# Performance work log

Measured on AMD Instinct MI355X. Metric: run time of the kernel, lower is better.

Reference implementation:

```python
import jax, jax.numpy as jnp
import numpy as np


def _fwd_diffs(x, D, scale):
    # forward difference along each of the first D axes, zero at the end, scaled by x.shape[0]
    outs = []
    for d in range(D):
        pad = [(0, 0)] * x.ndim
        pad[d] = (0, 1)
        outs.append(jnp.pad(jnp.diff(x, axis=d), pad) * scale)
    return jnp.stack(outs, 0)


def _bwd_diffs(p, scale):
    # p: [D, *dims, l]; backward difference of p[i] along axis i with the torch narrow/cat semantics
    outs = []
    for i in range(p.shape[0]):
        pi = p[i]
        head = jax.lax.slice_in_dim(pi, 0, pi.shape[i] - 1, axis=i)
        z = jnp.zeros_like(jax.lax.slice_in_dim(pi, 0, 1, axis=i))
        before = jnp.concatenate([head, z], axis=i)
        after = jnp.concatenate([z, head], axis=i)
        outs.append((before - after) * scale)
    return jnp.stack(outs, 0)


def _solver(f, repeats, l, lmbda, nu):
    dims = list(f.shape)
    H = dims[0]
    D = len(dims) - 1
    res = 1.0 / H
    tauu = res / 6.0
    sigmap = res / (3.0 + l)
    sigmas = 1.0
    proj = l * (l - 1) // 2 + l
    tau = 1.0 / (2.0 + proj / 4.0)
    # (k1,k2) interval combinations and the membership matrix M[K,z] = (k1<=z<=k2)
    combos = np.array([(a, b) for a in range(l) for b in range(a, l)], dtype=np.int32)
    k1 = jnp.asarray(combos[:, 0])
    k2 = jnp.asarray(combos[:, 1])
    zz = np.arange(l)
    M = jnp.asarray(((combos[:, :1] <= zz) & (zz <= combos[:, 1:2])).astype(np.float32))  # [proj, l]

    img = jnp.broadcast_to(f[..., None], tuple(dims) + (l,))
    klf = jnp.arange(1, l + 1, dtype=f.dtype) / l - img  # k/l - f
    u = img
    ubar = img
    px = jnp.zeros((D,) + tuple(dims) + (l,), f.dtype)
    pt = jnp.zeros(tuple(dims) + (l,), f.dtype)
    sx = jnp.zeros((D,) + tuple(dims) + (proj,), f.dtype)
    mux = sx
    mubarx = sx
    nrj = jnp.zeros((), f.dtype)
    h_un = u

    for it in range(int(repeats)):
        # ---- parabola: dual ascent on (px,pt) with closed-form cubic (Cardano) projection ----
        musum = jnp.einsum('...p,pz->...z', mux, M)
        ux = px + sigmap * (_fwd_diffs(ubar, D, H) + musum)
        ut = pt + sigmap * (jnp.pad(jnp.diff(ubar, axis=-1), [(0, 0)] * (ubar.ndim - 1) + [(0, 1)]) * l)
        pen = lmbda * klf * klf
        B = 0.25 * jnp.sum(ux * ux, axis=0) - pen
        mask = ut < B
        y = ut + pen
        norm = jnp.sqrt(jnp.sum(ux * ux, axis=0))
        a = 0.5 * norm                                   # 2*0.25*norm
        b = (2.0 / 3.0) * (1.0 - 0.5 * y)
        sb = jnp.sqrt(jnp.maximum(-b, 0.0))              # sqrt(-b), only used where b<0
        d = jnp.where(b < 0, (a - sb ** 3) * (a + sb ** 3), a * a + b ** 3)
        c = jnp.power(a + jnp.sqrt(jnp.maximum(d, 0.0)), 1.0 / 3.0)
        mask1 = (d >= 0) & (c == 0)
        mask3 = d < 0
        sb3 = jnp.where(sb > 0, sb ** 3, 1.0)
        ratio = jnp.clip(a / sb3, -1.0, 1.0)
        c_safe = jnp.where(c == 0, 1.0, c)
        v = jnp.where(mask1, 0.0,
                      jnp.where(mask3, 2.0 * sb * jnp.cos(jnp.arccos(ratio) / 3.0), c - b / c_safe))
        norm_safe = jnp.where(norm == 0, 1.0, norm)
        px = jnp.where(mask[None],
                       jnp.where((norm == 0)[None], 0.0, (2.0 * v / norm_safe)[None] * ux),
                       ux)
        pt = jnp.where(mask, 0.25 * jnp.sum(px * px, axis=0) - pen, ut)

        # ---- l2 projection of s ----
        mx = sx - sigmas * mubarx
        snorm = jnp.sqrt(jnp.sum(mx * mx, axis=0))
        snorm_safe = jnp.where(snorm == 0, 1.0, snorm)
        sx = jnp.where((snorm > nu * H)[None], mx * nu / snorm_safe[None], mx)

        # ---- mu update: per-(k1,k2) partial sums over the label axis via cumsum ----
        cs = jnp.cumsum(px, axis=-1)
        cs = jnp.pad(cs, [(0, 0)] * (px.ndim - 1) + [(1, 0)])
        t = cs[..., k2 + 1] - cs[..., k1]                # [D, *dims, proj]
        mux_new = mux + tau * (sx - t)
        mubarx = 2.0 * mux_new - mux
        mux = mux_new

        # ---- clipping: primal update with box projection and boundary conditions ----
        if it % 10 == 0:
            h_un = u
        dx = _bwd_diffs(px, H)
        head = pt[..., :-1]
        z = jnp.zeros_like(pt[..., :1])
        dt = (jnp.concatenate([head, z], axis=-1) - jnp.concatenate([z, head], axis=-1)) * l
        Dv = u + tauu * (jnp.sum(dx, axis=0) + dt)
        un = jnp.clip(Dv, 0.0, 1.0)
        un = un.at[..., 0].set(1.0).at[..., l - 1].set(0.0)
        ubar = 2.0 * un - u
        u = un
        if it % 10 == 0:
            nrj = jnp.sum(jnp.abs(u - h_un))
    return u, nrj


def setup_inputs() -> dict:
    key = jax.random.key(0)
    H, W = 256, 256
    f = jax.random.uniform(key, (H, W, 1), dtype=jnp.float32)
    return {"f": f, "repeats": 10, "l": 16, "lmbda": 0.5, "nu": 0.1, "tol": 0.0}


def reference(f, repeats, l, lmbda, nu, tol):
    # tol/early-exit: tol=0 so the torch break never fires; iteration count is fixed at `repeats`.
    u, nrj = _solver(f, repeats, l, lmbda, nu)
    denom = float(np.prod(f.shape[:-1])) * l
    return (u, nrj, nrj / denom, 0)
```

## Files before the change

### kernel.cpp

```cpp
#include <hip/hip_runtime.h>

#define HH 256
#define WW 256
#define NPIX (HH*WW)
#define LL 16
#define NL (NPIX*LL)
#define PP 136
#define PP2 (PP*2)

typedef _Float16 half_t;
typedef __attribute__((ext_vector_type(8))) _Float16 half8;

static constexpr float SIGMAP_F = (float)((1.0/256.0)/(3.0+16.0));
static constexpr float TAUU_F   = (float)((1.0/256.0)/6.0);
static constexpr float TAU_F    = (float)(1.0/36.0);

__device__ __forceinline__ float clampf(float x, float lo, float hi){
    return fminf(fmaxf(x, lo), hi);
}

template<int MODE>
__global__ __launch_bounds__(256) void k_prox(const float* __restrict__ f,
    const half_t* __restrict__ ubar,
    const half_t* __restrict__ pxOld,
    half_t* __restrict__ pxCur,
    half_t* __restrict__ pt,
    const half_t* __restrict__ musum,
    float* __restrict__ nrj)
{
    int tid = blockIdx.x*256 + threadIdx.x;
    if (MODE == 0 && tid == 0) *nrj = 0.0f;
    if (tid >= NL) return;
    int z = tid & (LL-1);
    int n = tid >> 4;
    int i = n >> 8;
    int j = n & (WW-1);

    float ux0, ux1, ut;
    float fv = f[n];
    if (MODE == 0) {
        float g0 = (i < HH-1) ? (f[n + WW] - fv) * 256.0f : 0.0f;
        float g1 = (j < WW-1) ? (f[n + 1]  - fv) * 256.0f : 0.0f;
        ux0 = SIGMAP_F * g0;
        ux1 = SIGMAP_F * g1;
        ut  = 0.0f;
    } else {
        float ub = (float)ubar[tid];
        float g0 = (i < HH-1) ? ((float)ubar[tid + WW*LL] - ub) * 256.0f : 0.0f;
        float g1 = (j < WW-1) ? ((float)ubar[tid + LL]    - ub) * 256.0f : 0.0f;
        float gt = (z < LL-1) ? ((float)ubar[tid + 1]     - ub) * 16.0f  : 0.0f;
        float ms0 = (float)musum[tid];
        float ms1 = (float)musum[NL + tid];
        ux0 = (float)pxOld[tid]      + SIGMAP_F * (g0 + ms0);
        ux1 = (float)pxOld[NL + tid] + SIGMAP_F * (g1 + ms1);
        ut  = (float)pt[tid]         + SIGMAP_F * gt;
    }

    float klf = (float)(z + 1) * 0.0625f - fv;
    float pen = 0.5f * klf * klf;

    float n2 = ux0*ux0 + ux1*ux1;
    float B  = 0.25f * n2 - pen;
    bool mask = ut < B;

    float px0 = ux0, px1 = ux1, ptn = ut;
    if (mask) {
        float y    = ut + pen;
        float norm = sqrtf(n2);
        float a    = 0.5f * norm;
        float b    = (2.0f/3.0f) * (1.0f - 0.5f*y);
        float v;
        if (b < 0.0f) {
            float sb  = sqrtf(-b);
            float sb3 = sb*sb*sb;
            float dd  = (a - sb3)*(a + sb3);
            if (dd < 0.0f) {
                float ratio = clampf(a / sb3, -1.0f, 1.0f);
                v = 2.0f * sb * cosf(acosf(ratio) * (1.0f/3.0f));
            } else {
                float c = cbrtf(a + sqrtf(dd));
                v = (c == 0.0f) ? 0.0f : (c - b/c);
            }
        } else {
            float dd = a*a + b*b*b;
            float c  = cbrtf(a + sqrtf(dd));
            v = (c == 0.0f) ? 0.0f : (c - b/c);
        }
        if (norm == 0.0f) { px0 = 0.0f; px1 = 0.0f; }
        else              { float s = 2.0f*v/norm; px0 = s*ux0; px1 = s*ux1; }
        ptn = 0.25f*(px0*px0 + px1*px1) - pen;
    }
    pxCur[tid]      = (half_t)px0;
    pxCur[NL + tid] = (half_t)px1;
    pt[tid]         = (half_t)ptn;
}

template<int H, int MODE>
__device__ __forceinline__ void do_set(int d, int n, int lane,
    half8 ph0, half8 ph1, half8 pp0, half8 pp1,
    const half_t* __restrict__ muC,
    half_t* __restrict__ muO,
    float* __restrict__ part)
{
    constexpr size_t setbase = (size_t)H * 17 * 2 * NPIX;
    const size_t vb   = setbase + (size_t)n*16 + (size_t)d*8;
    const size_t vb1  = vb + (size_t)16*NPIX;
    const size_t tail = setbase + (size_t)32*NPIX + (size_t)n*2 + (size_t)d;

    half8 mCv0, mCv1, mOv0, mOv1;
    float mCT = 0.0f, mOT = 0.0f;
    if (MODE >= 1) {
        mCv0 = *reinterpret_cast<const half8*>(&muC[vb]);
        mCv1 = *reinterpret_cast<const half8*>(&muC[vb1]);
        mCT  = (float)muC[tail];
    }
    if (MODE == 2) {
        mOv0 = *reinterpret_cast<const half8*>(&muO[vb]);
        mOv1 = *reinterpret_cast<const half8*>(&muO[vb1]);
        mOT  = (float)muO[tail];
    }

    half8 muo0, muo1;
    half_t muoT = (half_t)0.0f;

    float C[LL];
    #pragma unroll
    for (int q = 0; q < LL; ++q) C[q] = 0.0f;

    float tsum = 0.0f, tprev = 0.0f, rsA = 0.0f, rsB = 0.0f;
    #pragma unroll
    for (int q = 0; q < 17; ++q) {
        const int b = (q <= 15-H) ? H + q : q - 1;
        if (q == 0 || q == 16-H) { tsum = 0.0f; tprev = 0.0f; }
        tsum  += (b < 8) ? (float)ph0[b] : (float)ph1[b-8];

        float mn;
        if (MODE == 0) {
            mn = -TAU_F * tsum;
        } else {
            float mC, mO = 0.0f;
            if (q < 8)       { mC=(float)mCv0[q];   if (MODE==2) mO=(float)mOv0[q]; }
            else if (q < 16) { mC=(float)mCv1[q-8]; if (MODE==2) mO=(float)mOv1[q-8]; }
            else             { mC=mCT;              if (MODE==2) mO=mOT; }
            tprev += (b < 8) ? (float)pp0[b] : (float)pp1[b-8];

            float sxp = (mC - mO) * 36.0f + tprev;
            float mx  = sxp - (2.0f*mC - mO);
            float mo  = __shfl_xor(mx, 1);
            float snorm = sqrtf(mx*mx + mo*mo);
            if (snorm > 25.6f) mx *= 0.1f / snorm;
            mn = mC + TAU_F*(mx - tsum);
        }

        if (q < 8)       muo0[q]   = (half_t)mn;
        else if (q < 16) muo1[q-8] = (half_t)mn;
        else             muoT      = (half_t)mn;

        if (q <= 15-H) rsA += mn; else rsB += mn;
        C[b] += mn;
    }

    *reinterpret_cast<half8*>(&muO[vb])  = muo0;
    *reinterpret_cast<half8*>(&muO[vb1]) = muo1;
    muO[tail] = muoT;

    float m = 0.0f;
    #pragma unroll
    for (int z = 0; z < LL; ++z) {
        if (z == H)    m += rsA;
        if (z == 15-H) m += rsB;
        if (z >= 1)    m -= C[z-1];
        part[H*1024 + z*64 + lane] = m;
    }
}

template<int MODE>
__global__ __launch_bounds__(512, 4) void k_smu_u(
    const float* __restrict__ f,
    const half_t* __restrict__ pxCur,
    const half_t* __restrict__ pxOld,
    const half_t* __restrict__ pt,
    const half_t* __restrict__ muC,
    half_t* __restrict__ muO,
    half_t* __restrict__ musum,
    float* __restrict__ u, half_t* __restrict__ ubar,
    float* __restrict__ nrj)
{
    __shared__ float part[8192];
    __shared__ float wsum[8];

    int tid  = threadIdx.x;
    int wv   = tid >> 6;
    int lane = tid & 63;
    int pix  = lane >> 1;
    int d    = lane & 1;
    int n    = blockIdx.x*32 + pix;

    const half8* pv = reinterpret_cast<const half8*>(pxCur + (size_t)d*NL + (size_t)n*LL);
    half8 ph0 = pv[0], ph1 = pv[1];
    half8 pp0, pp1;
    if (MODE >= 1) {
        const half8* ppv = reinterpret_cast<const half8*>(pxOld + (size_t)d*NL + (size_t)n*LL);
        pp0 = ppv[0]; pp1 = ppv[1];
    }

    if      (wv == 0) do_set<0,MODE>(d,n,lane,ph0,ph1,pp0,pp1,muC,muO,part);
    else if (wv == 1) do_set<1,MODE>(d,n,lane,ph0,ph1,pp0,pp1,muC,muO,part);
    else if (wv == 2) do_set<2,MODE>(d,n,lane,ph0,ph1,pp0,pp1,muC,muO,part);
    else if (wv == 3) do_set<3,MODE>(d,n,lane,ph0,ph1,pp0,pp1,muC,muO,part);
    else if (wv == 4) do_set<4,MODE>(d,n,lane,ph0,ph1,pp0,pp1,muC,muO,part);
    else if (wv == 5) do_set<5,MODE>(d,n,lane,ph0,ph1,pp0,pp1,muC,muO,part);
    else if (wv == 6) do_set<6,MODE>(d,n,lane,ph0,ph1,pp0,pp1,muC,muO,part);
    else              do_set<7,MODE>(d,n,lane,ph0,ph1,pp0,pp1,muC,muO,part);

    __syncthreads();

    #pragma unroll
    for (int r = 0; r < 2; ++r) {
        int z2    = (tid >> 6) + r*8;
        int inner = tid & 63;
        float s = 0.0f;
        #pragma unroll
        for (int hh = 0; hh < 8; ++hh) s += part[hh*1024 + z2*64 + inner];
        int d2 = inner & 1, pix2 = inner >> 1;
        musum[(size_t)d2*NL + ((size_t)blockIdx.x*32 + pix2)*LL + z2] = (half_t)s;
    }

    {
        int t  = blockIdx.x*512 + tid;
        int z  = t & (LL-1);
        int n2 = t >> 4;
        int i2 = n2 >> 8;
        int j2 = n2 & (WW-1);

        float p0c = (float)pxCur[t];
        float p1c = (float)pxCur[NL + t];
        float d0 = ((i2 < HH-1) ? p0c : 0.0f) - ((i2 > 0) ? (float)pxCur[t - WW*LL] : 0.0f);
        float d1 = ((j2 < WW-1) ? p1c : 0.0f) - ((j2 > 0) ? (float)pxCur[NL + t - LL] : 0.0f);
        float ptc = (float)pt[t];
        float dt = ((z < LL-1) ? ptc : 0.0f) - ((z > 0) ? (float)pt[t - 1] : 0.0f);

        float uo = (MODE == 0) ? f[n2] : u[t];
        float Dv = uo + TAUU_F * ((d0 + d1) * 256.0f + dt * 16.0f);
        float un = clampf(Dv, 0.0f, 1.0f);
        if (z == 0)     un = 1.0f;
        if (z == LL-1)  un = 0.0f;
        u[t]    = un;
        ubar[t] = (half_t)(2.0f*un - uo);

        if (MODE == 0) {
            float v = fabsf(un - uo);
            #pragma unroll
            for (int off = 32; off > 0; off >>= 1) v += __shfl_down(v, off);
            if ((tid & 63) == 0) wsum[wv] = v;
            __syncthreads();
            if (tid == 0) {
                float s = 0.0f;
                #pragma unroll
                for (int q = 0; q < 8; ++q) s += wsum[q];
                atomicAdd(nrj, s);
            }
        }
    }
}

__global__ void k_final(const float* __restrict__ nrj, float* __restrict__ out_tail)
{
    if (threadIdx.x == 0) {
        float e = *nrj;
        out_tail[0] = e;
        out_tail[1] = e * (1.0f/1048576.0f);
        out_tail[2] = 0.0f;
    }
}

extern "C" void kernel_launch(void* const* d_in, const int* in_sizes, int n_in,
                              void* d_out, int out_size, void* d_ws, size_t ws_size,
                              hipStream_t stream)
{
    const float* f = (const float*)d_in[0];
    float* out = (float*)d_out;

    char* w = (char*)d_ws;
    size_t off = 0;
    auto allocf = [&](size_t nfloats) {
        float* p = (float*)(w + off);
        off += nfloats * sizeof(float);
        return p;
    };
    auto alloch = [&](size_t nhalf) {
        half_t* p = (half_t*)(w + off);
        off += nhalf * sizeof(half_t);
        return p;
    };
    half_t* muA    = alloch((size_t)NPIX * PP2);
    half_t* muB    = alloch((size_t)NPIX * PP2);
    half_t* musum  = alloch(2*(size_t)NL);
    half_t* pxA    = alloch(2*(size_t)NL);
    half_t* pxB    = alloch(2*(size_t)NL);
    half_t* pt     = alloch((size_t)NL);
    half_t* ubar   = alloch((size_t)NL);
    float*  u      = allocf((size_t)NL);
    float*  nrj    = allocf(64);
    (void)ws_size; (void)in_sizes; (void)n_in; (void)out_size;

    half_t* pxC = pxA;
    half_t* pxO = pxB;
    half_t* mC  = muA;
    half_t* mO  = muB;
    for (int it = 0; it < 10; ++it) {
        if (it == 0) {
            k_prox<0><<<NL/256, 256, 0, stream>>>(f, ubar, pxO, pxC, pt, musum, nrj);
            k_smu_u<0><<<NPIX/32, 512, 0, stream>>>(f, pxC, pxO, pt, mC, mO, musum, u, ubar, nrj);
        } else if (it == 1) {
            k_prox<1><<<NL/256, 256, 0, stream>>>(f, ubar, pxO, pxC, pt, musum, nrj);
            k_smu_u<1><<<NPIX/32, 512, 0, stream>>>(f, pxC, pxO, pt, mC, mO, musum, u, ubar, nrj);
        } else {
            k_prox<1><<<NL/256, 256, 0, stream>>>(f, ubar, pxO, pxC, pt, musum, nrj);
            k_smu_u<2><<<NPIX/32, 512, 0, stream>>>(f, pxC, pxO, pt, mC, mO, musum, u, ubar, nrj);
        }
        { half_t* tmp = pxC; pxC = pxO; pxO = tmp; }
        { half_t* tmp = mC;  mC  = mO;  mO  = tmp; }
    }

    hipMemcpyAsync(out, u, (size_t)NL*sizeof(float), hipMemcpyDeviceToDevice, stream);
    k_final<<<1, 64, 0, stream>>>(nrj, out + NL);
}
```

Measured before the change: 423.7 us.

## Vectorize prox kernel, restructure mu partial sums, hoist loads, drop final copy

The prox kernel now has each thread handle 8 labels, using half8 vector loads and stores instead of scalar accesses. The mu update drops the per-bin accumulator array and rebuilds the partial sums with suffix sums over the stored outputs. The primal-update loads are moved ahead of the barrier to overlap with the reduction, and the launch bound is raised to 8 blocks per SM. The last iteration writes straight to the output, removing the device-to-device memcpy. The changes cut memory transactions and a launch, but may raise register pressure and lower prox-kernel parallelism.

Result: slower. 819.8 us (+93.5%).

```diff
diff --git a/kernel.cpp b/kernel.cpp
--- a/kernel.cpp
+++ b/kernel.cpp
@@ -17,6 +17,12 @@
 
 __device__ __forceinline__ float clampf(float x, float lo, float hi){
     return fminf(fmaxf(x, lo), hi);
+}
+__device__ __forceinline__ half8 h8zero() {
+    half8 v;
+    #pragma unroll
+    for (int i = 0; i < 8; ++i) v[i] = (half_t)0.0f;
+    return v;
 }
 
 template<int MODE>
@@ -28,71 +34,97 @@
     const half_t* __restrict__ musum,
     float* __restrict__ nrj)
 {
-    int tid = blockIdx.x*256 + threadIdx.x;
-    if (MODE == 0 && tid == 0) *nrj = 0.0f;
-    if (tid >= NL) return;
-    int z = tid & (LL-1);
-    int n = tid >> 4;
-    int i = n >> 8;
-    int j = n & (WW-1);
-
-    float ux0, ux1, ut;
+    int t = blockIdx.x*256 + threadIdx.x;
+    if (MODE == 0 && t == 0) *nrj = 0.0f;
+    int n  = t >> 1;
+    int hf = t & 1;
+    int z0 = hf << 3;
+    int i = n >> 8, j = n & (WW-1);
+    bool iok = (i < HH-1), jok = (j < WW-1);
+    size_t base = (size_t)n*LL + z0;
+
     float fv = f[n];
+    float g0c = 0.0f, g1c = 0.0f;
+    half8 ubv = h8zero(), ubi = h8zero(), ubj = h8zero();
+    float ubz8 = 0.0f;
+    half8 ms0v = h8zero(), ms1v = h8zero();
+    half8 p0v  = h8zero(), p1v  = h8zero(), ptv = h8zero();
     if (MODE == 0) {
-        float g0 = (i < HH-1) ? (f[n + WW] - fv) * 256.0f : 0.0f;
-        float g1 = (j < WW-1) ? (f[n + 1]  - fv) * 256.0f : 0.0f;
-        ux0 = SIGMAP_F * g0;
-        ux1 = SIGMAP_F * g1;
-        ut  = 0.0f;
+        g0c = iok ? (f[n + WW] - fv) * 256.0f : 0.0f;
+        g1c = jok ? (f[n + 1]  - fv) * 256.0f : 0.0f;
     } else {
-        float ub = (float)ubar[tid];
-        float g0 = (i < HH-1) ? ((float)ubar[tid + WW*LL] - ub) * 256.0f : 0.0f;
-        float g1 = (j < WW-1) ? ((float)ubar[tid + LL]    - ub) * 256.0f : 0.0f;
-        float gt = (z < LL-1) ? ((float)ubar[tid + 1]     - ub) * 16.0f  : 0.0f;
-        float ms0 = (float)musum[tid];
-        float ms1 = (float)musum[NL + tid];
-        ux0 = (float)pxOld[tid]      + SIGMAP_F * (g0 + ms0);
-        ux1 = (float)pxOld[NL + tid] + SIGMAP_F * (g1 + ms1);
-        ut  = (float)pt[tid]         + SIGMAP_F * gt;
-    }
-
-    float klf = (float)(z + 1) * 0.0625f - fv;
-    float pen = 0.5f * klf * klf;
-
-    float n2 = ux0*ux0 + ux1*ux1;
-    float B  = 0.25f * n2 - pen;
-    bool mask = ut < B;
-
-    float px0 = ux0, px1 = ux1, ptn = ut;
-    if (mask) {
-        float y    = ut + pen;
-        float norm = sqrtf(n2);
-        float a    = 0.5f * norm;
-        float b    = (2.0f/3.0f) * (1.0f - 0.5f*y);
-        float v;
-        if (b < 0.0f) {
-            float sb  = sqrtf(-b);
-            float sb3 = sb*sb*sb;
-            float dd  = (a - sb3)*(a + sb3);
-            if (dd < 0.0f) {
-                float ratio = clampf(a / sb3, -1.0f, 1.0f);
-                v = 2.0f * sb * cosf(acosf(ratio) * (1.0f/3.0f));
+        ubv = *reinterpret_cast<const half8*>(ubar + base);
+        if (iok) ubi = *reinterpret_cast<const half8*>(ubar + base + (size_t)WW*LL);
+        if (jok) ubj = *reinterpret_cast<const half8*>(ubar + base + LL);
+        if (hf == 0) ubz8 = (float)ubar[base + 8];
+        ms0v = *reinterpret_cast<const half8*>(musum + base);
+        ms1v = *reinterpret_cast<const half8*>(musum + NL + base);
+        p0v  = *reinterpret_cast<const half8*>(pxOld + base);
+        p1v  = *reinterpret_cast<const half8*>(pxOld + NL + base);
+        ptv  = *reinterpret_cast<const half8*>(pt + base);
+    }
+
+    half8 o0, o1, opt;
+    #pragma unroll
+    for (int e = 0; e < 8; ++e) {
+        int z = z0 + e;
+        float ux0, ux1, ut;
+        if (MODE == 0) {
+            ux0 = SIGMAP_F * g0c;
+            ux1 = SIGMAP_F * g1c;
+            ut  = 0.0f;
+        } else {
+            float ub = (float)ubv[e];
+            float g0 = iok ? ((float)ubi[e] - ub) * 256.0f : 0.0f;
+            float g1 = jok ? ((float)ubj[e] - ub) * 256.0f : 0.0f;
+            float ubn = (e < 7) ? (float)ubv[e+1] : ubz8;
+            float gt = (z < LL-1) ? (ubn - ub) * 16.0f : 0.0f;
+            ux0 = (float)p0v[e] + SIGMAP_F * (g0 + (float)ms0v[e]);
+            ux1 = (float)p1v[e] + SIGMAP_F * (g1 + (float)ms1v[e]);
+            ut  = (float)ptv[e] + SIGMAP_F * gt;
+        }
+
+        float klf = (float)(z + 1) * 0.0625f - fv;
+        float pen = 0.5f * klf * klf;
+
+        float n2 = ux0*ux0 + ux1*ux1;
+        float B  = 0.25f * n2 - pen;
+        bool mask = ut < B;
+
+        float px0 = ux0, px1 = ux1, ptn = ut;
+        if (mask) {
+            float y    = ut + pen;
+            float norm = sqrtf(n2);
+            float a    = 0.5f * norm;
+            float b    = (2.0f/3.0f) * (1.0f - 0.5f*y);
+            float v;
+            if (b < 0.0f) {
+                float sb  = sqrtf(-b);
+                float sb3 = sb*sb*sb;
+                float dd  = (a - sb3)*(a + sb3);
+                if (dd < 0.0f) {
+                    float ratio = clampf(a / sb3, -1.0f, 1.0f);
+                    v = 2.0f * sb * cosf(acosf(ratio) * (1.0f/3.0f));
+                } else {
+                    float c = cbrtf(a + sqrtf(dd));
+                    v = (c == 0.0f) ? 0.0f : (c - b/c);
+                }
             } else {
-                float c = cbrtf(a + sqrtf(dd));
+                float dd = a*a + b*b*b;
+                float c  = cbrtf(a + sqrtf(dd));
                 v = (c == 0.0f) ? 0.0f : (c - b/c);
             }
-        } else {
-            float dd = a*a + b*b*b;
-            float c  = cbrtf(a + sqrtf(dd));
-            v = (c == 0.0f) ? 0.0f : (c - b/c);
-        }
-        if (norm == 0.0f) { px0 = 0.0f; px1 = 0.0f; }
-        else              { float s = 2.0f*v/norm; px0 = s*ux0; px1 = s*ux1; }
-        ptn = 0.25f*(px0*px0 + px1*px1) - pen;
-    }
-    pxCur[tid]      = (half_t)px0;
-    pxCur[NL + tid] = (half_t)px1;
-    pt[tid]         = (half_t)ptn;
+            if (norm == 0.0f) { px0 = 0.0f; px1 = 0.0f; }
+            else              { float s = 2.0f*v/norm; px0 = s*ux0; px1 = s*ux1; }
+            ptn = 0.25f*(px0*px0 + px1*px1) - pen;
+        }
+        o0[e]  = (half_t)px0;
+        o1[e]  = (half_t)px1;
+        opt[e] = (half_t)ptn;
+    }
+    *reinterpret_cast<half8*>(pxCur + base)      = o0;
+    *reinterpret_cast<half8*>(pxCur + NL + base) = o1;
+    *reinterpret_cast<half8*>(pt + base)         = opt;
 }
 
 template<int H, int MODE>
@@ -107,7 +139,7 @@
     const size_t vb1  = vb + (size_t)16*NPIX;
     const size_t tail = setbase + (size_t)32*NPIX + (size_t)n*2 + (size_t)d;
 
-    half8 mCv0, mCv1, mOv0, mOv1;
+    half8 mCv0 = h8zero(), mCv1 = h8zero(), mOv0 = h8zero(), mOv1 = h8zero();
     float mCT = 0.0f, mOT = 0.0f;
     if (MODE >= 1) {
         mCv0 = *reinterpret_cast<const half8*>(&muC[vb]);
@@ -123,59 +155,56 @@
     half8 muo0, muo1;
     half_t muoT = (half_t)0.0f;
 
-    float C[LL];
-    #pragma unroll
-    for (int q = 0; q < LL; ++q) C[q] = 0.0f;
-
-    float tsum = 0.0f, tprev = 0.0f, rsA = 0.0f, rsB = 0.0f;
+    float tsum = 0.0f, tprev = 0.0f;
     #pragma unroll
     for (int q = 0; q < 17; ++q) {
         const int b = (q <= 15-H) ? H + q : q - 1;
+        float mC, mO;
+        if (q < 8)       { mC=(float)mCv0[q];   mO=(float)mOv0[q]; }
+        else if (q < 16) { mC=(float)mCv1[q-8]; mO=(float)mOv1[q-8]; }
+        else             { mC=mCT;              mO=mOT; }
+
         if (q == 0 || q == 16-H) { tsum = 0.0f; tprev = 0.0f; }
         tsum  += (b < 8) ? (float)ph0[b] : (float)ph1[b-8];
-
-        float mn;
-        if (MODE == 0) {
-            mn = -TAU_F * tsum;
-        } else {
-            float mC, mO = 0.0f;
-            if (q < 8)       { mC=(float)mCv0[q];   if (MODE==2) mO=(float)mOv0[q]; }
-            else if (q < 16) { mC=(float)mCv1[q-8]; if (MODE==2) mO=(float)mOv1[q-8]; }
-            else             { mC=mCT;              if (MODE==2) mO=mOT; }
+        if (MODE >= 1)
             tprev += (b < 8) ? (float)pp0[b] : (float)pp1[b-8];
 
-            float sxp = (mC - mO) * 36.0f + tprev;
-            float mx  = sxp - (2.0f*mC - mO);
-            float mo  = __shfl_xor(mx, 1);
-            float snorm = sqrtf(mx*mx + mo*mo);
-            if (snorm > 25.6f) mx *= 0.1f / snorm;
-            mn = mC + TAU_F*(mx - tsum);
-        }
+        float sxp = (mC - mO) * 36.0f + tprev;
+        float mx  = sxp - (2.0f*mC - mO);
+        float mo  = __shfl_xor(mx, 1);
+        float snorm = sqrtf(mx*mx + mo*mo);
+        if (snorm > 25.6f) mx *= 0.1f / snorm;
+        float mn = mC + TAU_F*(mx - tsum);
 
         if (q < 8)       muo0[q]   = (half_t)mn;
         else if (q < 16) muo1[q-8] = (half_t)mn;
         else             muoT      = (half_t)mn;
-
-        if (q <= 15-H) rsA += mn; else rsB += mn;
-        C[b] += mn;
     }
 
     *reinterpret_cast<half8*>(&muO[vb])  = muo0;
     *reinterpret_cast<half8*>(&muO[vb1]) = muo1;
     muO[tail] = muoT;
 
-    float m = 0.0f;
-    #pragma unroll
-    for (int z = 0; z < LL; ++z) {
-        if (z == H)    m += rsA;
-        if (z == 15-H) m += rsB;
-        if (z >= 1)    m -= C[z-1];
+    float sA = 0.0f, sB = 0.0f;
+    #pragma unroll
+    for (int z = 15; z >= 0; --z) {
+        float m = 0.0f;
+        if (z >= H) {
+            const int q = z - H;
+            sA += (q < 8) ? (float)muo0[q] : (q < 16) ? (float)muo1[q-8] : (float)muoT;
+            m += sA;
+        }
+        if (z >= 15-H) {
+            const int q = z + 1;
+            sB += (q < 8) ? (float)muo0[q] : (q < 16) ? (float)muo1[q-8] : (float)muoT;
+            m += sB;
+        }
         part[H*1024 + z*64 + lane] = m;
     }
 }
 
 template<int MODE>
-__global__ __launch_bounds__(512, 4) void k_smu_u(
+__global__ __launch_bounds__(512, 8) void k_smu_u(
     const float* __restrict__ f,
     const half_t* __restrict__ pxCur,
     const half_t* __restrict__ pxOld,
@@ -184,7 +213,8 @@
     half_t* __restrict__ muO,
     half_t* __restrict__ musum,
     float* __restrict__ u, half_t* __restrict__ ubar,
-    float* __restrict__ nrj)
+    float* __restrict__ out,
+    float* __restrict__ nrj, int last)
 {
     __shared__ float part[8192];
     __shared__ float wsum[8];
@@ -198,7 +228,7 @@
 
     const half8* pv = reinterpret_cast<const half8*>(pxCur + (size_t)d*NL + (size_t)n*LL);
     half8 ph0 = pv[0], ph1 = pv[1];
-    half8 pp0, pp1;
+    half8 pp0 = h8zero(), pp1 = h8zero();
     if (MODE >= 1) {
         const half8* ppv = reinterpret_cast<const half8*>(pxOld + (size_t)d*NL + (size_t)n*LL);
         pp0 = ppv[0]; pp1 = ppv[1];
@@ -213,6 +243,19 @@
     else if (wv == 6) do_set<6,MODE>(d,n,lane,ph0,ph1,pp0,pp1,muC,muO,part);
     else              do_set<7,MODE>(d,n,lane,ph0,ph1,pp0,pp1,muC,muO,part);
 
+    int t  = blockIdx.x*512 + tid;
+    int z  = t & (LL-1);
+    int n2 = t >> 4;
+    int i2 = n2 >> 8;
+    int j2 = n2 & (WW-1);
+    float p0c = (float)pxCur[t];
+    float p1c = (float)pxCur[NL + t];
+    float p0u = (i2 > 0) ? (float)pxCur[t - WW*LL] : 0.0f;
+    float p1l = (j2 > 0) ? (float)pxCur[NL + t - LL] : 0.0f;
+    float ptc = (float)pt[t];
+    float ptm = (z > 0) ? (float)pt[t - 1] : 0.0f;
+    float uo  = (MODE == 0) ? f[n2] : u[t];
+
     __syncthreads();
 
     #pragma unroll
@@ -227,26 +270,19 @@
     }
 
     {
-        int t  = blockIdx.x*512 + tid;
-        int z  = t & (LL-1);
-        int n2 = t >> 4;
-        int i2 = n2 >> 8;
-        int j2 = n2 & (WW-1);
-
-        float p0c = (float)pxCur[t];
-        float p1c = (float)pxCur[NL + t];
-        float d0 = ((i2 < HH-1) ? p0c : 0.0f) - ((i2 > 0) ? (float)pxCur[t - WW*LL] : 0.0f);
-        float d1 = ((j2 < WW-1) ? p1c : 0.0f) - ((j2 > 0) ? (float)pxCur[NL + t - LL] : 0.0f);
-        float ptc = (float)pt[t];
-        float dt = ((z < LL-1) ? ptc : 0.0f) - ((z > 0) ? (float)pt[t - 1] : 0.0f);
-
-        float uo = (MODE == 0) ? f[n2] : u[t];
+        float d0 = ((i2 < HH-1) ? p0c : 0.0f) - p0u;
+        float d1 = ((j2 < WW-1) ? p1c : 0.0f) - p1l;
+        float dt = ((z < LL-1) ? ptc : 0.0f) - ptm;
+
         float Dv = uo + TAUU_F * ((d0 + d1) * 256.0f + dt * 16.0f);
         float un = clampf(Dv, 0.0f, 1.0f);
         if (z == 0)     un = 1.0f;
         if (z == LL-1)  un = 0.0f;
-        u[t]    = un;
-        ubar[t] = (half_t)(2.0f*un - uo);
+        if (last) out[t] = un;
+        else {
+            u[t]    = un;
+            ubar[t] = (half_t)(2.0f*un - uo);
+        }
 
         if (MODE == 0) {
             float v = fabsf(un - uo);
@@ -309,20 +345,20 @@
     half_t* mC  = muA;
     half_t* mO  = muB;
     for (int it = 0; it < 10; ++it) {
+        int last = (it == 9) ? 1 : 0;
         if (it == 0) {
-            k_prox<0><<<NL/256, 256, 0, stream>>>(f, ubar, pxO, pxC, pt, musum, nrj);
-            k_smu_u<0><<<NPIX/32, 512, 0, stream>>>(f, pxC, pxO, pt, mC, mO, musum, u, ubar, nrj);
+            k_prox<0><<<2*NPIX/256, 256, 0, stream>>>(f, ubar, pxO, pxC, pt, musum, nrj);
+            k_smu_u<0><<<NPIX/32, 512, 0, stream>>>(f, pxC, pxO, pt, mC, mO, musum, u, ubar, out, nrj, last);
         } else if (it == 1) {
-            k_prox<1><<<NL/256, 256, 0, stream>>>(f, ubar, pxO, pxC, pt, musum, nrj);
-            k_smu_u<1><<<NPIX/32, 512, 0, stream>>>(f, pxC, pxO, pt, mC, mO, musum, u, ubar, nrj);
+            k_prox<1><<<2*NPIX/256, 256, 0, stream>>>(f, ubar, pxO, pxC, pt, musum, nrj);
+            k_smu_u<1><<<NPIX/32, 512, 0, stream>>>(f, pxC, pxO, pt, mC, mO, musum, u, ubar, out, nrj, last);
         } else {
-            k_prox<1><<<NL/256, 256, 0, stream>>>(f, ubar, pxO, pxC, pt, musum, nrj);
-            k_smu_u<2><<<NPIX/32, 512, 0, stream>>>(f, pxC, pxO, pt, mC, mO, musum, u, ubar, nrj);
+            k_prox<1><<<2*NPIX/256, 256, 0, stream>>>(f, ubar, pxO, pxC, pt, musum, nrj);
+            k_smu_u<2><<<NPIX/32, 512, 0, stream>>>(f, pxC, pxO, pt, mC, mO, musum, u, ubar, out, nrj, last);
         }
         { half_t* tmp = pxC; pxC = pxO; pxO = tmp; }
         { half_t* tmp = mC;  mC  = mO;  mO  = tmp; }
     }
 
-    hipMemcpyAsync(out, u, (size_t)NL*sizeof(float), hipMemcpyDeviceToDevice, stream);
     k_final<<<1, 64, 0, stream>>>(nrj, out + NL);
 }
```
